# Optimization experiments

Hardware: AMD Instinct MI355X
Metric: run time of the kernel (lower is better)

The kernel has to match this reference:

```python
import jax, jax.numpy as jnp
import numpy as np

N, E, D = 20000, 640000, 128  # nodes, edges, hidden_nf
ED = 3  # edge_feat_nf (1 input col + distance col + geodesic col)
NORM_FACTOR = 100.0
NORM_CONST = 1.0
LN_EPS = 1e-5


def setup_inputs() -> dict:
    key = jax.random.key(0)
    ks = jax.random.split(key, 24)
    w = lambda k, s: (jax.random.normal(k, s, dtype=jnp.float32) * 0.1)
    inp = {
        "h": jax.random.normal(ks[0], (N, D), dtype=jnp.float32),
        "x": jax.random.normal(ks[1], (N, 3), dtype=jnp.float32),
        "edge_index": jax.random.randint(ks[2], (2, E), 0, N),
        "node_mask": jnp.ones((N, 1), jnp.float32),
        "edge_mask": jnp.ones((E, 1), jnp.float32),
        "edge_attr": jax.random.uniform(ks[3], (E, 1), dtype=jnp.float32),
        # GCLayer params
        "W_lin": w(ks[4], (D, D)), "b_lin": jnp.zeros((D,), jnp.float32),
        "We1": w(ks[5], (D + ED, D)), "be1": jnp.zeros((D,), jnp.float32),
        "We2": w(ks[6], (D, D)), "be2": jnp.zeros((D,), jnp.float32),
        "Wn1": w(ks[7], (D, D)), "bn1": jnp.zeros((D,), jnp.float32),
        "Wn2": w(ks[8], (D, D)), "bn2": jnp.zeros((D,), jnp.float32),
        "Wa1": w(ks[9], (2 * D + ED, D)), "ba1": jnp.zeros((D,), jnp.float32),
        "Wa2": w(ks[10], (D, 1)), "ba2": jnp.zeros((1,), jnp.float32),
        "ln_g": jnp.ones((D,), jnp.float32), "ln_b": jnp.zeros((D,), jnp.float32),
        # EquivariantUpdate coord_mlp params (last layer bias-free, gain 0.001)
        "Wc1": w(ks[11], (2 * D + ED, D)), "bc1": jnp.zeros((D,), jnp.float32),
        "Wc2": w(ks[12], (D, D)), "bc2": jnp.zeros((D,), jnp.float32),
        "Wc3": w(ks[13], (D, 1)) * 0.01,
    }
    return inp


def _forward(h, x, edge_index, node_mask, edge_mask, edge_attr,
             W_lin, b_lin, We1, be1, We2, be2, Wn1, bn1, Wn2, bn2,
             Wa1, ba1, Wa2, ba2, ln_g, ln_b, Wc1, bc1, Wc2, bc2, Wc3):
    silu = jax.nn.silu
    row, col = edge_index[0], edge_index[1]
    # coord2diff
    diff = x[row] - x[col]                                     # [E,3]
    radial = jnp.sum(diff * diff, axis=1, keepdims=True)
    dist = jnp.sqrt(radial + 1e-8)                             # [E,1]
    coord_diff = diff / (dist + NORM_CONST)
    e = jnp.concatenate([dist, edge_attr], axis=1)             # [E,2]
    # ---- GCLayer (Euclidean reduction of HGCLayer) ----
    hh = h @ W_lin + b_lin                                     # [N,D]
    hr, hc = hh[row], hh[col]
    geo = jnp.sqrt(jnp.sum((hr - hc) ** 2, axis=1, keepdims=True) + 1e-8)
    e3 = jnp.concatenate([e, geo], axis=1)                     # [E,3]
    att_in = jnp.concatenate([hr, hc, e3], axis=1)             # [E,2D+3]
    att = jax.nn.sigmoid(silu(att_in @ Wa1 + ba1) @ Wa2 + ba2) * edge_mask
    msg_in = jnp.concatenate([hc - hr, e3], axis=1)            # [E,D+3]
    msg = (silu(msg_in @ We1 + be1) @ We2 + be2) * att
    agg = jax.ops.segment_sum(msg, row, num_segments=hh.shape[0])  # [N,D]
    out = silu(agg @ Wn1 + bn1) @ Wn2 + bn2
    hh = hh + out
    mu = jnp.mean(hh, axis=-1, keepdims=True)
    var = jnp.mean((hh - mu) ** 2, axis=-1, keepdims=True)
    hh = (hh - mu) * jax.lax.rsqrt(var + LN_EPS) * ln_g + ln_b
    hh = silu(hh)
    # ---- EquivariantUpdate (tanh=False) ----
    cin = jnp.concatenate([hh[row], hh[col], e3], axis=1)      # [E,2D+3]
    m = silu(cin @ Wc1 + bc1)
    m = silu(m @ Wc2 + bc2)
    m = m @ Wc3                                                # [E,1]
    trans = coord_diff * m * edge_mask
    aggx = jax.ops.segment_sum(trans, row, num_segments=x.shape[0]) / NORM_FACTOR
    x_out = (x + aggx) * node_mask
    return hh, x_out


def reference(h, x, edge_index, node_mask, edge_mask, edge_attr,
              W_lin, b_lin, We1, be1, We2, be2, Wn1, bn1, Wn2, bn2,
              Wa1, ba1, Wa2, ba2, ln_g, ln_b, Wc1, bc1, Wc2, bc2, Wc3):
    return _forward(h, x, edge_index, node_mask, edge_mask, edge_attr,
                    W_lin, b_lin, We1, be1, We2, be2, Wn1, bn1, Wn2, bn2,
                    Wa1, ba1, Wa2, ba2, ln_g, ln_b, Wc1, bc1, Wc2, bc2, Wc3)
```

## Files before the change

### kernel.cpp

```cpp
#include <hip/hip_runtime.h>
#include <hip/hip_bf16.h>


#define D 128
#define RS 136

typedef unsigned short ushort;
typedef __fp16 half8 __attribute__((ext_vector_type(8)));
typedef __fp16 h16x2 __attribute__((ext_vector_type(2)));
typedef _Float16 f16x2 __attribute__((ext_vector_type(2)));
typedef __attribute__((ext_vector_type(4))) float f32x4;

__device__ __forceinline__ float rcpf(float x) { return __builtin_amdgcn_rcpf(x); }
__device__ __forceinline__ float siluf(float x) { return x * rcpf(1.0f + __expf(-x)); }
__device__ __forceinline__ float sigmf(float x) { return rcpf(1.0f + __expf(-x)); }
__device__ __forceinline__ ushort f2hs(float f) {
    _Float16 h = (_Float16)f; ushort u; __builtin_memcpy(&u, &h, 2); return u;
}
__device__ __forceinline__ unsigned pkh(float lo, float hi) {
    auto h = __builtin_amdgcn_cvt_pkrtz(lo, hi);
    unsigned u; __builtin_memcpy(&u, &h, 4); return u;
}
__device__ __forceinline__ float fdot2f(f16x2 a, f16x2 b, float c) {
#if __has_builtin(__builtin_amdgcn_fdot2)
    h16x2 ah, bh;
    __builtin_memcpy(&ah, &a, 4); __builtin_memcpy(&bh, &b, 4);
    return __builtin_amdgcn_fdot2(ah, bh, c, false);
#else
    return c + (float)a.x * (float)b.x + (float)a.y * (float)b.y;
#endif
}
#define MFMA16(a, b, c) __builtin_amdgcn_mfma_f32_16x16x32_f16((a), (b), (c), 0, 0, 0)

#define PWLIN 0
#define PWA1  5
#define PWE1  14
#define PWE2  19
#define PWN1  23
#define PWN2  28
#define PWC1  32
#define PWC2  41
#define NPACK 45

__global__ void k_zero(float* __restrict__ p, long n) {
    long i = (long)blockIdx.x * blockDim.x + threadIdx.x;
    long stride = (long)gridDim.x * blockDim.x;
    for (; i < n; i += stride) p[i] = 0.0f;
}

__global__ void k_hist(const int* __restrict__ eidx, int* __restrict__ cnt, int E) {
    int i = blockIdx.x * blockDim.x + threadIdx.x;
    const int stride = gridDim.x * blockDim.x;
    for (; i < E; i += stride) atomicAdd(&cnt[eidx[i]], 1);
}

__global__ __launch_bounds__(1024) void k_scan(const int* __restrict__ cnt,
                                               int* __restrict__ cur, int N) {
    __shared__ int part[1024];
    const int t = threadIdx.x;
    const int chunk = (N + 1023) / 1024;
    int s = 0;
    for (int k = 0; k < chunk; ++k) {
        const int i = t * chunk + k;
        if (i < N) s += cnt[i];
    }
    part[t] = s;
    __syncthreads();
    for (int d = 1; d < 1024; d <<= 1) {
        const int v = (t >= d) ? part[t - d] : 0;
        __syncthreads();
        part[t] += v;
        __syncthreads();
    }
    int base = (t == 0) ? 0 : part[t - 1];
    for (int k = 0; k < chunk; ++k) {
        const int i = t * chunk + k;
        if (i < N) { cur[i] = base; base += cnt[i]; }
    }
}

__global__ void k_scatter_build(
    const int* __restrict__ eidx, const float* __restrict__ x,
    const float* __restrict__ eattr, const float* __restrict__ emask,
    int* __restrict__ cur, float4* __restrict__ rec, int E) {
    int i = blockIdx.x * blockDim.x + threadIdx.x;
    const int stride = gridDim.x * blockDim.x;
    for (; i < E; i += stride) {
        const int r = eidx[i], c = eidx[E + i];
        const int p = atomicAdd(&cur[r], 1);
        const float dx = x[r * 3 + 0] - x[c * 3 + 0];
        const float dy = x[r * 3 + 1] - x[c * 3 + 1];
        const float dz = x[r * 3 + 2] - x[c * 3 + 2];
        const float dist = sqrtf(dx * dx + dy * dy + dz * dz + 1e-8f);
        const float inv = rcpf(dist + 1.0f);
        rec[2 * p + 0] = make_float4(__int_as_float(r), __int_as_float(c), dist, eattr[i]);
        rec[2 * p + 1] = make_float4(emask[i], dx * inv, dy * inv, dz * inv);
    }
}

__global__ __launch_bounds__(256) void k_packall(
    const float* __restrict__ W_lin, const float* __restrict__ b_lin,
    const float* __restrict__ Wa1, const float* __restrict__ ba1,
    const float* __restrict__ We1, const float* __restrict__ be1,
    const float* __restrict__ We2,
    const float* __restrict__ Wn1, const float* __restrict__ bn1,
    const float* __restrict__ Wn2,
    const float* __restrict__ Wc1, const float* __restrict__ bc1,
    const float* __restrict__ Wc2,
    ushort* __restrict__ pack) {
    const int b = blockIdx.x, t = threadIdx.x;
    const float* W = nullptr; const float* bias = nullptr;
    int kbase = 0, fold = 0, ext = 0, nW = 0;
    if (b < 5)       { W = W_lin; bias = b_lin; if (b == 4) { ext = 1; nW = 0; } else kbase = b * 32; }
    else if (b < 14) { int k = b - 5;  W = Wa1; bias = ba1; if (k == 8) { ext = 1; nW = 3; kbase = 256; } else { kbase = k * 32; fold = (k < 4); } }
    else if (b < 19) { int k = b - 14; W = We1; bias = be1; if (k == 4) { ext = 1; nW = 3; kbase = 128; } else kbase = k * 32; }
    else if (b < 23) { W = We2; kbase = (b - 19) * 32; }
    else if (b < 28) { int k = b - 23; W = Wn1; bias = bn1; if (k == 4) { ext = 1; nW = 0; } else kbase = k * 32; }
    else if (b < 32) { W = Wn2; kbase = (b - 28) * 32; }
    else if (b < 41) { int k = b - 32; W = Wc1; bias = bc1; if (k == 8) { ext = 1; nW = 3; kbase = 256; } else kbase = k * 32; }
    else             { W = Wc2; kbase = (b - 41) * 32; }
    ushort* dst = pack + (size_t)b * 4096;
#pragma unroll
    for (int i = 0; i < 16; ++i) {
        const int e = t + 256 * i;
        const int j = e & 7, lane = (e >> 3) & 63, nt = e >> 9;
        const int kl = (lane >> 4) * 8 + j;
        const int n = nt * 16 + (lane & 15);
        float v;
        if (!ext) {
            v = W[(kbase + kl) * D + n];
            if (fold) v += W[(kbase + kl + 128) * D + n];
        } else {
            v = (kl < nW) ? W[(kbase + kl) * D + n] : (kl == nW ? bias[n] : 0.0f);
        }
        dst[e] = f2hs(v);
    }
}

__global__ __launch_bounds__(256) void k_node_lin(
    const float* __restrict__ h, const ushort* __restrict__ pack,
    float* __restrict__ hh, ushort* __restrict__ hh1b, int N) {
    __shared__ ushort hs[64][RS];
    const int t = threadIdx.x, lane = t & 63, wave = t >> 6;
    const int quad = lane >> 4, l16 = lane & 15;
    const int mh = wave >> 1, nh = wave & 1;
    const int base = blockIdx.x * 64;

#pragma unroll
    for (int q = 0; q < 8; ++q) {
        const int f = t + 256 * q;
        const int row = f >> 5, c4 = (f & 31) << 2;
        const int node = base + row;
        float4 v = make_float4(0.f, 0.f, 0.f, 0.f);
        if (node < N) v = *(const float4*)(h + (size_t)node * D + c4);
        *(uint2*)&hs[row][c4] = make_uint2(pkh(v.x, v.y), pkh(v.z, v.w));
    }
    __syncthreads();

    half8 aext = (half8)0;
    if (quad == 0) aext[0] = (__fp16)1.0f;

    f32x4 acc[2][4] = {};
    const half8* pB = (const half8*)(pack + (size_t)PWLIN * 4096);
#pragma unroll
    for (int ks = 0; ks < 5; ++ks) {
        half8 bfr[4];
#pragma unroll
        for (int nt = 0; nt < 4; ++nt) bfr[nt] = pB[(ks * 8 + nh * 4 + nt) * 64 + lane];
#pragma unroll
        for (int mt = 0; mt < 2; ++mt) {
            const half8 a = (ks < 4) ? *(const half8*)&hs[mh * 32 + mt * 16 + l16][ks * 32 + quad * 8]
                                     : aext;
#pragma unroll
            for (int nt = 0; nt < 4; ++nt) acc[mt][nt] = MFMA16(a, bfr[nt], acc[mt][nt]);
        }
    }
#pragma unroll
    for (int mt = 0; mt < 2; ++mt)
#pragma unroll
        for (int reg = 0; reg < 4; ++reg) {
            const int g = base + mh * 32 + mt * 16 + quad * 4 + reg;
            if (g < N) {
#pragma unroll
                for (int nt = 0; nt < 4; ++nt) {
                    const int col = nh * 64 + nt * 16 + l16;
                    const float v = acc[mt][nt][reg];
                    hh[(size_t)g * D + col] = v;
                    hh1b[(size_t)g * D + col] = f2hs(v);
                }
            }
        }
}

__global__ __launch_bounds__(256, 4) void k_edge1(
    const float4* __restrict__ rec,
    const ushort* __restrict__ hh1b, const ushort* __restrict__ pack,
    const float* __restrict__ Wa2f, const float* __restrict__ ba2f,
    const float* __restrict__ be2f,
    float* __restrict__ agg, float* __restrict__ geo_c, int E) {
    __shared__ ushort ab_s[2][64][RS];
    __shared__ float dist_s[64], attr_s[64], geo_s[64], att_s[64], em_s[64];
    __shared__ int node_s[64], col_s[64];
    __shared__ float attp_s[4][64];

    float (*msg_s)[130] = (float(*)[130])&ab_s[0][0][0];

    const int t = threadIdx.x, lane = t & 63, w = t >> 6;
    const int quad = lane >> 4, l16 = lane & 15;
    const int base = blockIdx.x * 64;

    if (t < 64) {
        const int i = base + t;
        int r = 0, c = 0; float dist = 0.f, at = 0.f, emv = 0.f;
        if (i < E) {
            const float4 ra = rec[2 * i + 0];
            const float4 rb = rec[2 * i + 1];
            r = __float_as_int(ra.x); c = __float_as_int(ra.y);
            dist = ra.z; at = ra.w; emv = rb.x;
        }
        node_s[t] = r; col_s[t] = c;
        dist_s[t] = dist; attr_s[t] = at; em_s[t] = emv;
    }
    float wa2[2], b3[2];
#pragma unroll
    for (int nt = 0; nt < 2; ++nt) {
        const int col = w * 32 + nt * 16 + l16;
        wa2[nt] = Wa2f[col]; b3[nt] = be2f[col];
    }
    __syncthreads();

    {
        const int g = t >> 4;
#pragma unroll
        for (int it = 0; it < 4; ++it) {
            const int e = g * 4 + it;
            const uint4 vr = *(const uint4*)(hh1b + (size_t)node_s[e] * D + l16 * 8);
            const uint4 vc = *(const uint4*)(hh1b + (size_t)col_s[e] * D + l16 * 8);
            *(uint4*)&ab_s[0][e][l16 * 8] = vr;
            const unsigned* pr = (const unsigned*)&vr;
            const unsigned* pc = (const unsigned*)&vc;
            float s = 0.f; unsigned dw[4];
#pragma unroll
            for (int q = 0; q < 4; ++q) {
                f16x2 hr2, hc2;
                __builtin_memcpy(&hr2, &pr[q], 4);
                __builtin_memcpy(&hc2, &pc[q], 4);
                const f16x2 d2 = hc2 - hr2;
                __builtin_memcpy(&dw[q], &d2, 4);
                s = fdot2f(d2, d2, s);
            }
            *(uint4*)&ab_s[1][e][l16 * 8] = make_uint4(dw[0], dw[1], dw[2], dw[3]);
            s += __shfl_xor(s, 1); s += __shfl_xor(s, 2); s += __shfl_xor(s, 4); s += __shfl_xor(s, 8);
            if (l16 == 0) {
                const float gg = sqrtf(s + 1e-8f);
                geo_s[e] = gg;
                if (base + e < E) geo_c[base + e] = gg;
            }
        }
    }
    __syncthreads();

    half8 aext[4];
#pragma unroll
    for (int mt = 0; mt < 4; ++mt) {
        half8 v = (half8)0;
        if (quad == 0) {
            const int m = mt * 16 + l16;
            v[0] = (__fp16)dist_s[m]; v[1] = (__fp16)attr_s[m];
            v[2] = (__fp16)geo_s[m];  v[3] = (__fp16)1.0f;
        }
        aext[mt] = v;
    }

    f32x4 accA[4][2] = {}, accM[4][2] = {};
    {
        const half8* pA = (const half8*)(pack + (size_t)PWA1 * 4096);
        const half8* pM = (const half8*)(pack + (size_t)PWE1 * 4096);
#pragma unroll
        for (int ks = 0; ks < 9; ++ks) {
            const half8 bA0 = pA[(ks * 8 + w * 2 + 0) * 64 + lane];
            const half8 bA1 = pA[(ks * 8 + w * 2 + 1) * 64 + lane];
            half8 bM0 = (half8)0, bM1 = (half8)0;
            if (ks >= 4) {
                bM0 = pM[((ks - 4) * 8 + w * 2 + 0) * 64 + lane];
                bM1 = pM[((ks - 4) * 8 + w * 2 + 1) * 64 + lane];
            }
#pragma unroll
            for (int mt = 0; mt < 4; ++mt) {
                const half8 a = (ks < 4) ? *(const half8*)&ab_s[0][mt * 16 + l16][ks * 32 + quad * 8]
                              : (ks < 8) ? *(const half8*)&ab_s[1][mt * 16 + l16][(ks - 4) * 32 + quad * 8]
                                         : aext[mt];
                accA[mt][0] = MFMA16(a, bA0, accA[mt][0]);
                accA[mt][1] = MFMA16(a, bA1, accA[mt][1]);
                if (ks >= 4) {
                    accM[mt][0] = MFMA16(a, bM0, accM[mt][0]);
                    accM[mt][1] = MFMA16(a, bM1, accM[mt][1]);
                }
            }
        }
    }
#pragma unroll
    for (int mt = 0; mt < 4; ++mt)
#pragma unroll
        for (int reg = 0; reg < 4; ++reg) {
            float p = siluf(accA[mt][0][reg]) * wa2[0] + siluf(accA[mt][1][reg]) * wa2[1];
            p += __shfl_xor(p, 1); p += __shfl_xor(p, 2); p += __shfl_xor(p, 4); p += __shfl_xor(p, 8);
            if (l16 == 0) attp_s[w][mt * 16 + quad * 4 + reg] = p;
        }
    __syncthreads();

    if (t < 64)
        att_s[t] = sigmf(attp_s[0][t] + attp_s[1][t] + attp_s[2][t] + attp_s[3][t] + ba2f[0]) * em_s[t];
#pragma unroll
    for (int mt = 0; mt < 4; ++mt)
#pragma unroll
        for (int reg = 0; reg < 4; ++reg) {
            const int row = mt * 16 + quad * 4 + reg;
#pragma unroll
            for (int nt = 0; nt < 2; ++nt)
                ab_s[0][row][w * 32 + nt * 16 + l16] = f2hs(siluf(accM[mt][nt][reg]));
        }
    __syncthreads();

    f32x4 acc3[4][2] = {};
    {
        const half8* pB = (const half8*)(pack + (size_t)PWE2 * 4096);
#pragma unroll
        for (int ks = 0; ks < 4; ++ks) {
            const half8 b0 = pB[(ks * 8 + w * 2 + 0) * 64 + lane];
            const half8 b1 = pB[(ks * 8 + w * 2 + 1) * 64 + lane];
#pragma unroll
            for (int mt = 0; mt < 4; ++mt) {
                const half8 a = *(const half8*)&ab_s[0][mt * 16 + l16][ks * 32 + quad * 8];
                acc3[mt][0] = MFMA16(a, b0, acc3[mt][0]);
                acc3[mt][1] = MFMA16(a, b1, acc3[mt][1]);
            }
        }
    }
    __syncthreads();
#pragma unroll
    for (int mt = 0; mt < 4; ++mt)
#pragma unroll
        for (int reg = 0; reg < 4; ++reg) {
            const int row = mt * 16 + quad * 4 + reg;
            const float av = att_s[row];
#pragma unroll
            for (int nt = 0; nt < 2; ++nt)
                msg_s[row][w * 32 + nt * 16 + l16] = (acc3[mt][nt][reg] + b3[nt]) * av;
        }
    __syncthreads();

    {
        const int j = t & 127, h = t >> 7;
        const int r0 = node_s[h * 32];
        if (r0 == node_s[h * 32 + 31]) {
            float acc = 0.f;
#pragma unroll
            for (int k = 0; k < 32; ++k) acc += msg_s[h * 32 + k][j];
            atomicAdd(&agg[(size_t)r0 * D + j], acc);
        } else {
            float acc = 0.f;
            int rprev = r0;
#pragma unroll
            for (int k = 0; k < 32; ++k) {
                const int row = h * 32 + k;
                const int rn = node_s[row];
                if (rn != rprev) {
                    atomicAdd(&agg[(size_t)rprev * D + j], acc);
                    acc = 0.f; rprev = rn;
                }
                acc += msg_s[row][j];
            }
            atomicAdd(&agg[(size_t)rprev * D + j], acc);
        }
    }
}

__global__ __launch_bounds__(256) void k_node2(
    const float* __restrict__ agg, float* hio,
    const ushort* __restrict__ pack,
    const float* __restrict__ bn2f,
    const float* __restrict__ ln_g, const float* __restrict__ ln_b,
    ushort* __restrict__ hh2b, int N) {
    __shared__ ushort ag_s[64][RS];
    __shared__ float redS[2][64], redQ[2][64];
    const int t = threadIdx.x, lane = t & 63, wave = t >> 6;
    const int quad = lane >> 4, l16 = lane & 15;
    const int mh = wave >> 1, nh = wave & 1;
    const int base = blockIdx.x * 64;

#pragma unroll
    for (int q = 0; q < 8; ++q) {
        const int f = t + 256 * q;
        const int row = f >> 5, c4 = (f & 31) << 2;
        const int node = base + row;
        float4 v = make_float4(0.f, 0.f, 0.f, 0.f);
        if (node < N) v = *(const float4*)(agg + (size_t)node * D + c4);
        *(uint2*)&ag_s[row][c4] = make_uint2(pkh(v.x, v.y), pkh(v.z, v.w));
    }
    float bn2[4], lg[4], lb[4];
#pragma unroll
    for (int nt = 0; nt < 4; ++nt) {
        const int col = nh * 64 + nt * 16 + l16;
        bn2[nt] = bn2f[col]; lg[nt] = ln_g[col]; lb[nt] = ln_b[col];
    }
    __syncthreads();

    half8 aext = (half8)0;
    if (quad == 0) aext[0] = (__fp16)1.0f;

    f32x4 acc[2][4] = {};
    {
        const half8* pB = (const half8*)(pack + (size_t)PWN1 * 4096);
#pragma unroll
        for (int ks = 0; ks < 5; ++ks) {
            half8 bfr[4];
#pragma unroll
            for (int nt = 0; nt < 4; ++nt) bfr[nt] = pB[(ks * 8 + nh * 4 + nt) * 64 + lane];
#pragma unroll
            for (int mt = 0; mt < 2; ++mt) {
                const half8 a = (ks < 4) ? *(const half8*)&ag_s[mh * 32 + mt * 16 + l16][ks * 32 + quad * 8]
                                         : aext;
#pragma unroll
                for (int nt = 0; nt < 4; ++nt) acc[mt][nt] = MFMA16(a, bfr[nt], acc[mt][nt]);
            }
        }
    }
    __syncthreads();
#pragma unroll
    for (int mt = 0; mt < 2; ++mt)
#pragma unroll
        for (int reg = 0; reg < 4; ++reg) {
            const int row = mh * 32 + mt * 16 + quad * 4 + reg;
#pragma unroll
            for (int nt = 0; nt < 4; ++nt)
                ag_s[row][nh * 64 + nt * 16 + l16] = f2hs(siluf(acc[mt][nt][reg]));
        }
    __syncthreads();

    {
        const half8* pB = (const half8*)(pack + (size_t)PWN2 * 4096);
#pragma unroll
        for (int mt = 0; mt < 2; ++mt)
#pragma unroll
            for (int nt = 0; nt < 4; ++nt) acc[mt][nt] = (f32x4)0.0f;
#pragma unroll
        for (int ks = 0; ks < 4; ++ks) {
            half8 bfr[4];
#pragma unroll
            for (int nt = 0; nt < 4; ++nt) bfr[nt] = pB[(ks * 8 + nh * 4 + nt) * 64 + lane];
#pragma unroll
            for (int mt = 0; mt < 2; ++mt) {
                const half8 a = *(const half8*)&ag_s[mh * 32 + mt * 16 + l16][ks * 32 + quad * 8];
#pragma unroll
                for (int nt = 0; nt < 4; ++nt) acc[mt][nt] = MFMA16(a, bfr[nt], acc[mt][nt]);
            }
        }
    }
#pragma unroll
    for (int mt = 0; mt < 2; ++mt)
#pragma unroll
        for (int reg = 0; reg < 4; ++reg) {
            const int row = mh * 32 + mt * 16 + quad * 4 + reg;
            const int g = base + row;
            float s = 0.f, qq = 0.f;
#pragma unroll
            for (int nt = 0; nt < 4; ++nt) {
                const int col = nh * 64 + nt * 16 + l16;
                float v = acc[mt][nt][reg] + bn2[nt];
                if (g < N) v += hio[(size_t)g * D + col];
                acc[mt][nt][reg] = v;
                s += v; qq += v * v;
            }
            s += __shfl_xor(s, 1); s += __shfl_xor(s, 2); s += __shfl_xor(s, 4); s += __shfl_xor(s, 8);
            qq += __shfl_xor(qq, 1); qq += __shfl_xor(qq, 2); qq += __shfl_xor(qq, 4); qq += __shfl_xor(qq, 8);
            if (l16 == 0) { redS[nh][row] = s; redQ[nh][row] = qq; }
        }
    __syncthreads();

#pragma unroll
    for (int mt = 0; mt < 2; ++mt)
#pragma unroll
        for (int reg = 0; reg < 4; ++reg) {
            const int row = mh * 32 + mt * 16 + quad * 4 + reg;
            const int g = base + row;
            const float mu = (redS[0][row] + redS[1][row]) * (1.0f / D);
            const float var = (redQ[0][row] + redQ[1][row]) * (1.0f / D) - mu * mu;
            const float rstd = rsqrtf(var + 1e-5f);
            if (g < N) {
#pragma unroll
                for (int nt = 0; nt < 4; ++nt) {
                    const int col = nh * 64 + nt * 16 + l16;
                    const float hn = (acc[mt][nt][reg] - mu) * rstd * lg[nt] + lb[nt];
                    const float o = siluf(hn);
                    hio[(size_t)g * D + col] = o;
                    hh2b[(size_t)g * D + col] = f2hs(o);
                }
            }
        }
}

__global__ __launch_bounds__(256, 4) void k_edge2(
    const float4* __restrict__ rec, const float* __restrict__ geo_c,
    const ushort* __restrict__ hh2b, const ushort* __restrict__ pack,
    const float* __restrict__ bc2f, const float* __restrict__ Wc3f,
    float* __restrict__ aggx, int E) {
    __shared__ ushort ar_s[64][RS];
    __shared__ ushort ac_s[64][RS];
    __shared__ float dist_s[64], attr_s[64], geo_s[64], tr_s[64];
    __shared__ float cdx_s[64], cdy_s[64], cdz_s[64];
    __shared__ int node_s[64], col_s[64];
    __shared__ float mp_s[4][64];

    const int t = threadIdx.x, lane = t & 63, w = t >> 6;
    const int quad = lane >> 4, l16 = lane & 15;
    const int base = blockIdx.x * 64;

    if (t < 64) {
        const int i = base + t;
        int r = 0, c = 0;
        float dist = 1.f, geo = 0.f, at = 0.f, emv = 0.f, cdx = 0.f, cdy = 0.f, cdz = 0.f;
        if (i < E) {
            const float4 ra = rec[2 * i + 0];
            const float4 rb = rec[2 * i + 1];
            r = __float_as_int(ra.x); c = __float_as_int(ra.y);
            dist = ra.z; at = ra.w;
            emv = rb.x; cdx = rb.y; cdy = rb.z; cdz = rb.w;
            geo = geo_c[i];
        }
        node_s[t] = r; col_s[t] = c;
        dist_s[t] = dist; geo_s[t] = geo; attr_s[t] = at; tr_s[t] = emv;
        cdx_s[t] = cdx; cdy_s[t] = cdy; cdz_s[t] = cdz;
    }
    float bc2[2], wc3[2];
#pragma unroll
    for (int nt = 0; nt < 2; ++nt) {
        const int col = w * 32 + nt * 16 + l16;
        bc2[nt] = bc2f[col]; wc3[nt] = Wc3f[col];
    }
    __syncthreads();

    {
        const int g = t >> 4;
#pragma unroll
        for (int it = 0; it < 4; ++it) {
            const int e = g * 4 + it;
            *(uint4*)&ar_s[e][l16 * 8] = *(const uint4*)(hh2b + (size_t)node_s[e] * D + l16 * 8);
            *(uint4*)&ac_s[e][l16 * 8] = *(const uint4*)(hh2b + (size_t)col_s[e] * D + l16 * 8);
        }
    }
    __syncthreads();

    half8 aext[4];
#pragma unroll
    for (int mt = 0; mt < 4; ++mt) {
        half8 v = (half8)0;
        if (quad == 0) {
            const int m = mt * 16 + l16;
            v[0] = (__fp16)dist_s[m]; v[1] = (__fp16)attr_s[m];
            v[2] = (__fp16)geo_s[m];  v[3] = (__fp16)1.0f;
        }
        aext[mt] = v;
    }

    {
        f32x4 acc[4][2] = {};
        const half8* pB = (const half8*)(pack + (size_t)PWC1 * 4096);
#pragma unroll
        for (int ks = 0; ks < 9; ++ks) {
            const half8 b0 = pB[(ks * 8 + w * 2 + 0) * 64 + lane];
            const half8 b1 = pB[(ks * 8 + w * 2 + 1) * 64 + lane];
#pragma unroll
            for (int mt = 0; mt < 4; ++mt) {
                const half8 a = (ks < 4) ? *(const half8*)&ar_s[mt * 16 + l16][ks * 32 + quad * 8]
                              : (ks < 8) ? *(const half8*)&ac_s[mt * 16 + l16][(ks - 4) * 32 + quad * 8]
                                         : aext[mt];
                acc[mt][0] = MFMA16(a, b0, acc[mt][0]);
                acc[mt][1] = MFMA16(a, b1, acc[mt][1]);
            }
        }
        __syncthreads();
#pragma unroll
        for (int mt = 0; mt < 4; ++mt)
#pragma unroll
            for (int reg = 0; reg < 4; ++reg) {
                const int row = mt * 16 + quad * 4 + reg;
#pragma unroll
                for (int nt = 0; nt < 2; ++nt)
                    ar_s[row][w * 32 + nt * 16 + l16] = f2hs(siluf(acc[mt][nt][reg]));
            }
    }
    __syncthreads();

    {
        f32x4 acc[4][2] = {};
        const half8* pB = (const half8*)(pack + (size_t)PWC2 * 4096);
#pragma unroll
        for (int ks = 0; ks < 4; ++ks) {
            const half8 b0 = pB[(ks * 8 + w * 2 + 0) * 64 + lane];
            const half8 b1 = pB[(ks * 8 + w * 2 + 1) * 64 + lane];
#pragma unroll
            for (int mt = 0; mt < 4; ++mt) {
                const half8 a = *(const half8*)&ar_s[mt * 16 + l16][ks * 32 + quad * 8];
                acc[mt][0] = MFMA16(a, b0, acc[mt][0]);
                acc[mt][1] = MFMA16(a, b1, acc[mt][1]);
            }
        }
#pragma unroll
        for (int mt = 0; mt < 4; ++mt)
#pragma unroll
            for (int reg = 0; reg < 4; ++reg) {
                float p = siluf(acc[mt][0][reg] + bc2[0]) * wc3[0]
                        + siluf(acc[mt][1][reg] + bc2[1]) * wc3[1];
                p += __shfl_xor(p, 1); p += __shfl_xor(p, 2); p += __shfl_xor(p, 4); p += __shfl_xor(p, 8);
                if (l16 == 0) mp_s[w][mt * 16 + quad * 4 + reg] = p;
            }
    }
    __syncthreads();

    if (t < 64) {
        const float m = mp_s[0][t] + mp_s[1][t] + mp_s[2][t] + mp_s[3][t];
        tr_s[t] = m * tr_s[t];
        if (base + t >= E) tr_s[t] = 0.f;
    }
    __syncthreads();

    {
        const int h = t >> 7, tt = t & 127;
        if (tt < 3) {
            const float* cds = (tt == 0) ? cdx_s : (tt == 1) ? cdy_s : cdz_s;
            float acc = 0.f;
            int rprev = node_s[h * 32];
#pragma unroll
            for (int k = 0; k < 32; ++k) {
                const int row = h * 32 + k;
                const int rn = node_s[row];
                if (rn != rprev) {
                    atomicAdd(&aggx[rprev * 4 + tt], acc);
                    acc = 0.f; rprev = rn;
                }
                acc += cds[row] * tr_s[row];
            }
            atomicAdd(&aggx[rprev * 4 + tt], acc);
        }
    }
}

__global__ void k_coord(const float* __restrict__ x, const float* __restrict__ nmask,
                        const float* __restrict__ aggx, float* __restrict__ out_x, int N) {
    const int idx = blockIdx.x * blockDim.x + threadIdx.x;
    if (idx >= N * 3) return;
    const int i = idx / 3, d = idx - i * 3;
    out_x[idx] = (x[idx] + aggx[i * 4 + d] * (1.0f / 100.0f)) * nmask[i];
}

extern "C" void kernel_launch(void* const* d_in, const int* in_sizes, int n_in,
                              void* d_out, int out_size, void* d_ws, size_t ws_size,
                              hipStream_t stream) {
    const float* h     = (const float*)d_in[0];
    const float* x     = (const float*)d_in[1];
    const int*   eidx  = (const int*)d_in[2];
    const float* nmask = (const float*)d_in[3];
    const float* emask = (const float*)d_in[4];
    const float* eattr = (const float*)d_in[5];
    const float* W_lin = (const float*)d_in[6];
    const float* b_lin = (const float*)d_in[7];
    const float* We1   = (const float*)d_in[8];
    const float* be1   = (const float*)d_in[9];
    const float* We2   = (const float*)d_in[10];
    const float* be2   = (const float*)d_in[11];
    const float* Wn1   = (const float*)d_in[12];
    const float* bn1   = (const float*)d_in[13];
    const float* Wn2   = (const float*)d_in[14];
    const float* bn2   = (const float*)d_in[15];
    const float* Wa1   = (const float*)d_in[16];
    const float* ba1   = (const float*)d_in[17];
    const float* Wa2   = (const float*)d_in[18];
    const float* ba2   = (const float*)d_in[19];
    const float* ln_g  = (const float*)d_in[20];
    const float* ln_b  = (const float*)d_in[21];
    const float* Wc1   = (const float*)d_in[22];
    const float* bc1   = (const float*)d_in[23];
    const float* Wc2   = (const float*)d_in[24];
    const float* bc2   = (const float*)d_in[25];
    const float* Wc3   = (const float*)d_in[26];

    const int N = in_sizes[0] / D;
    const int E = in_sizes[2] / 2;

    char* wp = (char*)d_ws;
    auto take = [&](size_t bytes) -> void* {
        void* p = wp; wp += (bytes + 255) & ~(size_t)255; return p;
    };
    float*  agg   = (float*)take((size_t)N * D * 4);
    float*  aggx  = (float*)take((size_t)N * 4 * 4);
    int*    cnt   = (int*)take((size_t)N * 4);
    int*    cur   = (int*)take((size_t)N * 4);
    float4* rec   = (float4*)take((size_t)E * 32);
    float*  geo_c = (float*)take((size_t)E * 4);
    ushort* hh1b  = (ushort*)take((size_t)N * D * 2);
    ushort* hh2b  = (ushort*)take((size_t)N * D * 2);
    ushort* pack  = (ushort*)take((size_t)NPACK * 4096 * 2);

    float* out_h = (float*)d_out;
    float* out_x = out_h + (size_t)N * D;

    const int EB = (E + 63) / 64;
    const int NB = (N + 63) / 64;
    const long zn = ((char*)(cnt + N) - (char*)agg) / 4;

    k_zero<<<2048, 256, 0, stream>>>(agg, zn);
    k_packall<<<NPACK, 256, 0, stream>>>(W_lin, b_lin, Wa1, ba1, We1, be1, We2,
                                         Wn1, bn1, Wn2, Wc1, bc1, Wc2, pack);
    k_hist<<<1024, 256, 0, stream>>>(eidx, cnt, E);
    k_scan<<<1, 1024, 0, stream>>>(cnt, cur, N);
    k_scatter_build<<<1024, 256, 0, stream>>>(eidx, x, eattr, emask, cur, rec, E);
    k_node_lin<<<NB, 256, 0, stream>>>(h, pack, out_h, hh1b, N);
    k_edge1<<<EB, 256, 0, stream>>>(rec, hh1b, pack, Wa2, ba2, be2, agg, geo_c, E);
    k_node2<<<NB, 256, 0, stream>>>(agg, out_h, pack, bn2, ln_g, ln_b, hh2b, N);
    k_edge2<<<EB, 256, 0, stream>>>(rec, geo_c, hh2b, pack, bc2, Wc3, aggx, E);
    k_coord<<<(N * 3 + 255) / 256, 256, 0, stream>>>(x, nmask, aggx, out_x, N);
}
```

Baseline: 535.9 us.

## Hoist first-layer edge matmuls to per-node projections gathered per edge

The first linear layers of the edge attention, edge message and coordinate MLPs are split by linearity into per-node projections (U, V, M for edge1 and P, Q for edge2), computed once per node in the node kernels with MFMA. The edge kernels then gather those projected rows, add the small edge-feature terms from weights staged in shared memory, and apply the activation, so the large per-edge K=256+ matmuls are replaced by elementwise work. This moves matmul FLOPs from E edges to N nodes, at the cost of extra node-side outputs, more gather bandwidth (several fp16/fp32 rows per edge), and extra fp16 rounding of differences. Occupancy hints for the edge kernels are raised to 6 blocks per SM.

```diff
diff --git a/kernel.cpp b/kernel.cpp
--- a/kernel.cpp
+++ b/kernel.cpp
@@ -20,6 +20,14 @@
 __device__ __forceinline__ unsigned pkh(float lo, float hi) {
     auto h = __builtin_amdgcn_cvt_pkrtz(lo, hi);
     unsigned u; __builtin_memcpy(&u, &h, 4); return u;
+}
+__device__ __forceinline__ unsigned pksub(unsigned a, unsigned b) {
+    f16x2 x, y; __builtin_memcpy(&x, &a, 4); __builtin_memcpy(&y, &b, 4);
+    f16x2 d = x - y; unsigned r; __builtin_memcpy(&r, &d, 4); return r;
+}
+__device__ __forceinline__ float2 up2(unsigned u) {
+    f16x2 h; __builtin_memcpy(&h, &u, 4);
+    return make_float2((float)h.x, (float)h.y);
 }
 __device__ __forceinline__ float fdot2f(f16x2 a, f16x2 b, float c) {
 #if __has_builtin(__builtin_amdgcn_fdot2)
@@ -33,14 +41,16 @@
 #define MFMA16(a, b, c) __builtin_amdgcn_mfma_f32_16x16x32_f16((a), (b), (c), 0, 0, 0)
 
 #define PWLIN 0
-#define PWA1  5
-#define PWE1  14
-#define PWE2  19
-#define PWN1  23
-#define PWN2  28
-#define PWC1  32
-#define PWC2  41
-#define NPACK 45
+#define PU    5
+#define PV    9
+#define PM    13
+#define PE2   17
+#define PN1   21
+#define PN2   26
+#define PP    30
+#define PQ    34
+#define PC2   38
+#define NPACK 42
 
 __global__ void k_zero(float* __restrict__ p, long n) {
     long i = (long)blockIdx.x * blockDim.x + threadIdx.x;
@@ -100,25 +110,27 @@
 
 __global__ __launch_bounds__(256) void k_packall(
     const float* __restrict__ W_lin, const float* __restrict__ b_lin,
-    const float* __restrict__ Wa1, const float* __restrict__ ba1,
-    const float* __restrict__ We1, const float* __restrict__ be1,
+    const float* __restrict__ Wa1,
+    const float* __restrict__ We1,
     const float* __restrict__ We2,
     const float* __restrict__ Wn1, const float* __restrict__ bn1,
     const float* __restrict__ Wn2,
-    const float* __restrict__ Wc1, const float* __restrict__ bc1,
+    const float* __restrict__ Wc1,
     const float* __restrict__ Wc2,
     ushort* __restrict__ pack) {
     const int b = blockIdx.x, t = threadIdx.x;
     const float* W = nullptr; const float* bias = nullptr;
     int kbase = 0, fold = 0, ext = 0, nW = 0;
     if (b < 5)       { W = W_lin; bias = b_lin; if (b == 4) { ext = 1; nW = 0; } else kbase = b * 32; }
-    else if (b < 14) { int k = b - 5;  W = Wa1; bias = ba1; if (k == 8) { ext = 1; nW = 3; kbase = 256; } else { kbase = k * 32; fold = (k < 4); } }
-    else if (b < 19) { int k = b - 14; W = We1; bias = be1; if (k == 4) { ext = 1; nW = 3; kbase = 128; } else kbase = k * 32; }
-    else if (b < 23) { W = We2; kbase = (b - 19) * 32; }
-    else if (b < 28) { int k = b - 23; W = Wn1; bias = bn1; if (k == 4) { ext = 1; nW = 0; } else kbase = k * 32; }
-    else if (b < 32) { W = Wn2; kbase = (b - 28) * 32; }
-    else if (b < 41) { int k = b - 32; W = Wc1; bias = bc1; if (k == 8) { ext = 1; nW = 3; kbase = 256; } else kbase = k * 32; }
-    else             { W = Wc2; kbase = (b - 41) * 32; }
+    else if (b < 9)  { W = Wa1; kbase = (b - 5) * 32; fold = 1; }
+    else if (b < 13) { W = Wa1; kbase = 128 + (b - 9) * 32; }
+    else if (b < 17) { W = We1; kbase = (b - 13) * 32; }
+    else if (b < 21) { W = We2; kbase = (b - 17) * 32; }
+    else if (b < 26) { int k = b - 21; W = Wn1; bias = bn1; if (k == 4) { ext = 1; nW = 0; } else kbase = k * 32; }
+    else if (b < 30) { W = Wn2; kbase = (b - 26) * 32; }
+    else if (b < 34) { W = Wc1; kbase = (b - 30) * 32; }
+    else if (b < 38) { W = Wc1; kbase = 128 + (b - 34) * 32; }
+    else             { W = Wc2; kbase = (b - 38) * 32; }
     ushort* dst = pack + (size_t)b * 4096;
 #pragma unroll
     for (int i = 0; i < 16; ++i) {
@@ -139,7 +151,9 @@
 
 __global__ __launch_bounds__(256) void k_node_lin(
     const float* __restrict__ h, const ushort* __restrict__ pack,
-    float* __restrict__ hh, ushort* __restrict__ hh1b, int N) {
+    float* __restrict__ hh, ushort* __restrict__ hh1b,
+    float* __restrict__ Uf, ushort* __restrict__ Vh, ushort* __restrict__ Mh,
+    const float* __restrict__ ba1f, int N) {
     __shared__ ushort hs[64][RS];
     const int t = threadIdx.x, lane = t & 63, wave = t >> 6;
     const int quad = lane >> 4, l16 = lane & 15;
@@ -155,55 +169,150 @@
         if (node < N) v = *(const float4*)(h + (size_t)node * D + c4);
         *(uint2*)&hs[row][c4] = make_uint2(pkh(v.x, v.y), pkh(v.z, v.w));
     }
+    float ba1v[4];
+#pragma unroll
+    for (int nt = 0; nt < 4; ++nt) ba1v[nt] = ba1f[nh * 64 + nt * 16 + l16];
     __syncthreads();
 
     half8 aext = (half8)0;
     if (quad == 0) aext[0] = (__fp16)1.0f;
 
     f32x4 acc[2][4] = {};
-    const half8* pB = (const half8*)(pack + (size_t)PWLIN * 4096);
-#pragma unroll
-    for (int ks = 0; ks < 5; ++ks) {
-        half8 bfr[4];
-#pragma unroll
-        for (int nt = 0; nt < 4; ++nt) bfr[nt] = pB[(ks * 8 + nh * 4 + nt) * 64 + lane];
-#pragma unroll
-        for (int mt = 0; mt < 2; ++mt) {
-            const half8 a = (ks < 4) ? *(const half8*)&hs[mh * 32 + mt * 16 + l16][ks * 32 + quad * 8]
-                                     : aext;
-#pragma unroll
-            for (int nt = 0; nt < 4; ++nt) acc[mt][nt] = MFMA16(a, bfr[nt], acc[mt][nt]);
-        }
-    }
+    {
+        const half8* pB = (const half8*)(pack + (size_t)PWLIN * 4096);
+#pragma unroll
+        for (int ks = 0; ks < 5; ++ks) {
+            half8 bfr[4];
+#pragma unroll
+            for (int nt = 0; nt < 4; ++nt) bfr[nt] = pB[(ks * 8 + nh * 4 + nt) * 64 + lane];
+#pragma unroll
+            for (int mt = 0; mt < 2; ++mt) {
+                const half8 a = (ks < 4) ? *(const half8*)&hs[mh * 32 + mt * 16 + l16][ks * 32 + quad * 8]
+                                         : aext;
+#pragma unroll
+                for (int nt = 0; nt < 4; ++nt) acc[mt][nt] = MFMA16(a, bfr[nt], acc[mt][nt]);
+            }
+        }
+    }
+    __syncthreads();
 #pragma unroll
     for (int mt = 0; mt < 2; ++mt)
 #pragma unroll
         for (int reg = 0; reg < 4; ++reg) {
-            const int g = base + mh * 32 + mt * 16 + quad * 4 + reg;
-            if (g < N) {
-#pragma unroll
-                for (int nt = 0; nt < 4; ++nt) {
-                    const int col = nh * 64 + nt * 16 + l16;
-                    const float v = acc[mt][nt][reg];
+            const int row = mh * 32 + mt * 16 + quad * 4 + reg;
+            const int g = base + row;
+#pragma unroll
+            for (int nt = 0; nt < 4; ++nt) {
+                const int col = nh * 64 + nt * 16 + l16;
+                const float v = acc[mt][nt][reg];
+                const ushort hv = f2hs(v);
+                hs[row][col] = hv;
+                if (g < N) {
                     hh[(size_t)g * D + col] = v;
-                    hh1b[(size_t)g * D + col] = f2hs(v);
+                    hh1b[(size_t)g * D + col] = hv;
                 }
             }
         }
-}
-
-__global__ __launch_bounds__(256, 4) void k_edge1(
+    __syncthreads();
+
+    {
+        f32x4 a2[2][4] = {};
+        const half8* pB = (const half8*)(pack + (size_t)PU * 4096);
+#pragma unroll
+        for (int ks = 0; ks < 4; ++ks) {
+            half8 bfr[4];
+#pragma unroll
+            for (int nt = 0; nt < 4; ++nt) bfr[nt] = pB[(ks * 8 + nh * 4 + nt) * 64 + lane];
+#pragma unroll
+            for (int mt = 0; mt < 2; ++mt) {
+                const half8 a = *(const half8*)&hs[mh * 32 + mt * 16 + l16][ks * 32 + quad * 8];
+#pragma unroll
+                for (int nt = 0; nt < 4; ++nt) a2[mt][nt] = MFMA16(a, bfr[nt], a2[mt][nt]);
+            }
+        }
+#pragma unroll
+        for (int mt = 0; mt < 2; ++mt)
+#pragma unroll
+            for (int reg = 0; reg < 4; ++reg) {
+                const int g = base + mh * 32 + mt * 16 + quad * 4 + reg;
+                if (g < N)
+#pragma unroll
+                    for (int nt = 0; nt < 4; ++nt)
+                        Uf[(size_t)g * D + nh * 64 + nt * 16 + l16] = a2[mt][nt][reg] + ba1v[nt];
+            }
+    }
+    {
+        f32x4 a2[2][4] = {};
+        const half8* pB = (const half8*)(pack + (size_t)PV * 4096);
+#pragma unroll
+        for (int ks = 0; ks < 4; ++ks) {
+            half8 bfr[4];
+#pragma unroll
+            for (int nt = 0; nt < 4; ++nt) bfr[nt] = pB[(ks * 8 + nh * 4 + nt) * 64 + lane];
+#pragma unroll
+            for (int mt = 0; mt < 2; ++mt) {
+                const half8 a = *(const half8*)&hs[mh * 32 + mt * 16 + l16][ks * 32 + quad * 8];
+#pragma unroll
+                for (int nt = 0; nt < 4; ++nt) a2[mt][nt] = MFMA16(a, bfr[nt], a2[mt][nt]);
+            }
+        }
+#pragma unroll
+        for (int mt = 0; mt < 2; ++mt)
+#pragma unroll
+            for (int reg = 0; reg < 4; ++reg) {
+                const int g = base + mh * 32 + mt * 16 + quad * 4 + reg;
+                if (g < N)
+#pragma unroll
+                    for (int nt = 0; nt < 4; ++nt)
+                        Vh[(size_t)g * D + nh * 64 + nt * 16 + l16] = f2hs(a2[mt][nt][reg]);
+            }
+    }
+    {
+        f32x4 a2[2][4] = {};
+        const half8* pB = (const half8*)(pack + (size_t)PM * 4096);
+#pragma unroll
+        for (int ks = 0; ks < 4; ++ks) {
+            half8 bfr[4];
+#pragma unroll
+            for (int nt = 0; nt < 4; ++nt) bfr[nt] = pB[(ks * 8 + nh * 4 + nt) * 64 + lane];
+#pragma unroll
+            for (int mt = 0; mt < 2; ++mt) {
+                const half8 a = *(const half8*)&hs[mh * 32 + mt * 16 + l16][ks * 32 + quad * 8];
+#pragma unroll
+                for (int nt = 0; nt < 4; ++nt) a2[mt][nt] = MFMA16(a, bfr[nt], a2[mt][nt]);
+            }
+        }
+#pragma unroll
+        for (int mt = 0; mt < 2; ++mt)
+#pragma unroll
+            for (int reg = 0; reg < 4; ++reg) {
+                const int g = base + mh * 32 + mt * 16 + quad * 4 + reg;
+                if (g < N)
+#pragma unroll
+                    for (int nt = 0; nt < 4; ++nt)
+                        Mh[(size_t)g * D + nh * 64 + nt * 16 + l16] = f2hs(a2[mt][nt][reg]);
+            }
+    }
+}
+
+__global__ __launch_bounds__(256, 6) void k_edge1(
     const float4* __restrict__ rec,
-    const ushort* __restrict__ hh1b, const ushort* __restrict__ pack,
+    const ushort* __restrict__ hh1b,
+    const float*  __restrict__ Uf,
+    const ushort* __restrict__ Vh,
+    const ushort* __restrict__ Mh,
+    const ushort* __restrict__ pack,
+    const float* __restrict__ Wa1, const float* __restrict__ We1,
+    const float* __restrict__ be1f,
     const float* __restrict__ Wa2f, const float* __restrict__ ba2f,
     const float* __restrict__ be2f,
     float* __restrict__ agg, float* __restrict__ geo_c, int E) {
-    __shared__ ushort ab_s[2][64][RS];
+    __shared__ ushort m1_s[64][RS];
+    __shared__ float ew_s[7][128];
     __shared__ float dist_s[64], attr_s[64], geo_s[64], att_s[64], em_s[64];
     __shared__ int node_s[64], col_s[64];
-    __shared__ float attp_s[4][64];
-
-    float (*msg_s)[130] = (float(*)[130])&ab_s[0][0][0];
+
+    float (*msg_s)[RS] = (float(*)[RS])&m1_s[0][0];
 
     const int t = threadIdx.x, lane = t & 63, w = t >> 6;
     const int quad = lane >> 4, l16 = lane & 15;
@@ -221,12 +330,17 @@
         node_s[t] = r; col_s[t] = c;
         dist_s[t] = dist; attr_s[t] = at; em_s[t] = emv;
     }
-    float wa2[2], b3[2];
-#pragma unroll
-    for (int nt = 0; nt < 2; ++nt) {
-        const int col = w * 32 + nt * 16 + l16;
-        wa2[nt] = Wa2f[col]; b3[nt] = be2f[col];
-    }
+    for (int i = t; i < 896; i += 256) {
+        const int r = i >> 7, c = i & 127;
+        float v;
+        if (r < 3)      v = Wa1[(256 + r) * D + c];
+        else if (r < 6) v = We1[(128 + (r - 3)) * D + c];
+        else            v = be1f[c];
+        ew_s[r][c] = v;
+    }
+    float b3[2];
+#pragma unroll
+    for (int nt = 0; nt < 2; ++nt) b3[nt] = be2f[w * 32 + nt * 16 + l16];
     __syncthreads();
 
     {
@@ -236,20 +350,17 @@
             const int e = g * 4 + it;
             const uint4 vr = *(const uint4*)(hh1b + (size_t)node_s[e] * D + l16 * 8);
             const uint4 vc = *(const uint4*)(hh1b + (size_t)col_s[e] * D + l16 * 8);
-            *(uint4*)&ab_s[0][e][l16 * 8] = vr;
             const unsigned* pr = (const unsigned*)&vr;
             const unsigned* pc = (const unsigned*)&vc;
-            float s = 0.f; unsigned dw[4];
+            float s = 0.f;
 #pragma unroll
             for (int q = 0; q < 4; ++q) {
                 f16x2 hr2, hc2;
                 __builtin_memcpy(&hr2, &pr[q], 4);
                 __builtin_memcpy(&hc2, &pc[q], 4);
                 const f16x2 d2 = hc2 - hr2;
-                __builtin_memcpy(&dw[q], &d2, 4);
                 s = fdot2f(d2, d2, s);
             }
-            *(uint4*)&ab_s[1][e][l16 * 8] = make_uint4(dw[0], dw[1], dw[2], dw[3]);
             s += __shfl_xor(s, 1); s += __shfl_xor(s, 2); s += __shfl_xor(s, 4); s += __shfl_xor(s, 8);
             if (l16 == 0) {
                 const float gg = sqrtf(s + 1e-8f);
@@ -260,119 +371,100 @@
     }
     __syncthreads();
 
-    half8 aext[4];
-#pragma unroll
-    for (int mt = 0; mt < 4; ++mt) {
-        half8 v = (half8)0;
-        if (quad == 0) {
-            const int m = mt * 16 + l16;
-            v[0] = (__fp16)dist_s[m]; v[1] = (__fp16)attr_s[m];
-            v[2] = (__fp16)geo_s[m];  v[3] = (__fp16)1.0f;
-        }
-        aext[mt] = v;
-    }
-
-    f32x4 accA[4][2] = {}, accM[4][2] = {};
-    {
-        const half8* pA = (const half8*)(pack + (size_t)PWA1 * 4096);
-        const half8* pM = (const half8*)(pack + (size_t)PWE1 * 4096);
-#pragma unroll
-        for (int ks = 0; ks < 9; ++ks) {
-            const half8 bA0 = pA[(ks * 8 + w * 2 + 0) * 64 + lane];
-            const half8 bA1 = pA[(ks * 8 + w * 2 + 1) * 64 + lane];
-            half8 bM0 = (half8)0, bM1 = (half8)0;
-            if (ks >= 4) {
-                bM0 = pM[((ks - 4) * 8 + w * 2 + 0) * 64 + lane];
-                bM1 = pM[((ks - 4) * 8 + w * 2 + 1) * 64 + lane];
-            }
-#pragma unroll
-            for (int mt = 0; mt < 4; ++mt) {
-                const half8 a = (ks < 4) ? *(const half8*)&ab_s[0][mt * 16 + l16][ks * 32 + quad * 8]
-                              : (ks < 8) ? *(const half8*)&ab_s[1][mt * 16 + l16][(ks - 4) * 32 + quad * 8]
-                                         : aext[mt];
-                accA[mt][0] = MFMA16(a, bA0, accA[mt][0]);
-                accA[mt][1] = MFMA16(a, bA1, accA[mt][1]);
-                if (ks >= 4) {
-                    accM[mt][0] = MFMA16(a, bM0, accM[mt][0]);
-                    accM[mt][1] = MFMA16(a, bM1, accM[mt][1]);
-                }
-            }
-        }
-    }
-#pragma unroll
-    for (int mt = 0; mt < 4; ++mt)
-#pragma unroll
-        for (int reg = 0; reg < 4; ++reg) {
-            float p = siluf(accA[mt][0][reg]) * wa2[0] + siluf(accA[mt][1][reg]) * wa2[1];
-            p += __shfl_xor(p, 1); p += __shfl_xor(p, 2); p += __shfl_xor(p, 4); p += __shfl_xor(p, 8);
-            if (l16 == 0) attp_s[w][mt * 16 + quad * 4 + reg] = p;
-        }
-    __syncthreads();
-
-    if (t < 64)
-        att_s[t] = sigmf(attp_s[0][t] + attp_s[1][t] + attp_s[2][t] + attp_s[3][t] + ba2f[0]) * em_s[t];
-#pragma unroll
-    for (int mt = 0; mt < 4; ++mt)
-#pragma unroll
-        for (int reg = 0; reg < 4; ++reg) {
-            const int row = mt * 16 + quad * 4 + reg;
-#pragma unroll
-            for (int nt = 0; nt < 2; ++nt)
-                ab_s[0][row][w * 32 + nt * 16 + l16] = f2hs(siluf(accM[mt][nt][reg]));
-        }
+    {
+        const int row = t >> 2, cq = t & 3;
+        const int nr = node_s[row], nc = col_s[row];
+        const float dist = dist_s[row], attr = attr_s[row], geo = geo_s[row];
+        const float*  pU  = Uf + (size_t)nr * D + cq * 32;
+        const ushort* pVr = Vh + (size_t)nr * D + cq * 32;
+        const ushort* pVc = Vh + (size_t)nc * D + cq * 32;
+        const ushort* pMr = Mh + (size_t)nr * D + cq * 32;
+        const ushort* pMc = Mh + (size_t)nc * D + cq * 32;
+        float p = 0.f;
+#pragma unroll
+        for (int k4 = 0; k4 < 8; ++k4) {
+            const int c4 = cq * 32 + k4 * 4;
+            const float4 u  = *(const float4*)(pU + k4 * 4);
+            const uint2 vru = *(const uint2*)(pVr + k4 * 4);
+            const uint2 vcu = *(const uint2*)(pVc + k4 * 4);
+            const uint2 mru = *(const uint2*)(pMr + k4 * 4);
+            const uint2 mcu = *(const uint2*)(pMc + k4 * 4);
+            const float2 vd01 = up2(pksub(vcu.x, vru.x));
+            const float2 vd23 = up2(pksub(vcu.y, vru.y));
+            const float2 md01 = up2(pksub(mcu.x, mru.x));
+            const float2 md23 = up2(pksub(mcu.y, mru.y));
+            const float4 e0 = *(const float4*)&ew_s[0][c4];
+            const float4 e1 = *(const float4*)&ew_s[1][c4];
+            const float4 e2 = *(const float4*)&ew_s[2][c4];
+            const float4 f0 = *(const float4*)&ew_s[3][c4];
+            const float4 f1 = *(const float4*)&ew_s[4][c4];
+            const float4 f2 = *(const float4*)&ew_s[5][c4];
+            const float4 bb = *(const float4*)&ew_s[6][c4];
+            const float4 w2 = *(const float4*)(Wa2f + c4);
+            const float a0 = u.x + vd01.x + dist * e0.x + attr * e1.x + geo * e2.x;
+            const float a1 = u.y + vd01.y + dist * e0.y + attr * e1.y + geo * e2.y;
+            const float a2 = u.z + vd23.x + dist * e0.z + attr * e1.z + geo * e2.z;
+            const float a3 = u.w + vd23.y + dist * e0.w + attr * e1.w + geo * e2.w;
+            p += siluf(a0) * w2.x + siluf(a1) * w2.y + siluf(a2) * w2.z + siluf(a3) * w2.w;
+            const float m0 = siluf(md01.x + dist * f0.x + attr * f1.x + geo * f2.x + bb.x);
+            const float m1v = siluf(md01.y + dist * f0.y + attr * f1.y + geo * f2.y + bb.y);
+            const float m2 = siluf(md23.x + dist * f0.z + attr * f1.z + geo * f2.z + bb.z);
+            const float m3 = siluf(md23.y + dist * f0.w + attr * f1.w + geo * f2.w + bb.w);
+            *(uint2*)&m1_s[row][c4] = make_uint2(pkh(m0, m1v), pkh(m2, m3));
+        }
+        p += __shfl_xor(p, 1); p += __shfl_xor(p, 2);
+        if (cq == 0) att_s[row] = sigmf(p + ba2f[0]) * em_s[row];
+    }
     __syncthreads();
 
     f32x4 acc3[4][2] = {};
     {
-        const half8* pB = (const half8*)(pack + (size_t)PWE2 * 4096);
+        const half8* pB = (const half8*)(pack + (size_t)PE2 * 4096);
 #pragma unroll
         for (int ks = 0; ks < 4; ++ks) {
             const half8 b0 = pB[(ks * 8 + w * 2 + 0) * 64 + lane];
             const half8 b1 = pB[(ks * 8 + w * 2 + 1) * 64 + lane];
 #pragma unroll
             for (int mt = 0; mt < 4; ++mt) {
-                const half8 a = *(const half8*)&ab_s[0][mt * 16 + l16][ks * 32 + quad * 8];
+                const half8 a = *(const half8*)&m1_s[mt * 16 + l16][ks * 32 + quad * 8];
                 acc3[mt][0] = MFMA16(a, b0, acc3[mt][0]);
                 acc3[mt][1] = MFMA16(a, b1, acc3[mt][1]);
             }
         }
     }
     __syncthreads();
-#pragma unroll
-    for (int mt = 0; mt < 4; ++mt)
-#pragma unroll
-        for (int reg = 0; reg < 4; ++reg) {
-            const int row = mt * 16 + quad * 4 + reg;
-            const float av = att_s[row];
-#pragma unroll
-            for (int nt = 0; nt < 2; ++nt)
-                msg_s[row][w * 32 + nt * 16 + l16] = (acc3[mt][nt][reg] + b3[nt]) * av;
-        }
-    __syncthreads();
-
-    {
-        const int j = t & 127, h = t >> 7;
-        const int r0 = node_s[h * 32];
-        if (r0 == node_s[h * 32 + 31]) {
+
+#pragma unroll
+    for (int pass = 0; pass < 2; ++pass) {
+#pragma unroll
+        for (int mt = 0; mt < 2; ++mt)
+#pragma unroll
+            for (int reg = 0; reg < 4; ++reg) {
+                const int row = (pass * 2 + mt) * 16 + quad * 4 + reg;
+                const float av = att_s[row];
+#pragma unroll
+                for (int nt = 0; nt < 2; ++nt)
+                    msg_s[row - pass * 32][w * 32 + nt * 16 + l16] =
+                        (acc3[pass * 2 + mt][nt][reg] + b3[nt]) * av;
+            }
+        __syncthreads();
+        {
+            const int j = t & 127, s = t >> 7;
+            const int r0 = pass * 32 + s * 16;
             float acc = 0.f;
-#pragma unroll
-            for (int k = 0; k < 32; ++k) acc += msg_s[h * 32 + k][j];
-            atomicAdd(&agg[(size_t)r0 * D + j], acc);
-        } else {
-            float acc = 0.f;
-            int rprev = r0;
-#pragma unroll
-            for (int k = 0; k < 32; ++k) {
-                const int row = h * 32 + k;
-                const int rn = node_s[row];
+            int rprev = node_s[r0];
+#pragma unroll
+            for (int k = 0; k < 16; ++k) {
+                const int rn = node_s[r0 + k];
                 if (rn != rprev) {
                     atomicAdd(&agg[(size_t)rprev * D + j], acc);
                     acc = 0.f; rprev = rn;
                 }
-                acc += msg_s[row][j];
+                acc += msg_s[s * 16 + k][j];
             }
             atomicAdd(&agg[(size_t)rprev * D + j], acc);
         }
+        __syncthreads();
     }
 }
 
@@ -381,7 +473,8 @@
     const ushort* __restrict__ pack,
     const float* __restrict__ bn2f,
     const float* __restrict__ ln_g, const float* __restrict__ ln_b,
-    ushort* __restrict__ hh2b, int N) {
+    const float* __restrict__ bc1f,
+    ushort* __restrict__ Ph, ushort* __restrict__ Qh, int N) {
     __shared__ ushort ag_s[64][RS];
     __shared__ float redS[2][64], redQ[2][64];
     const int t = threadIdx.x, lane = t & 63, wave = t >> 6;
@@ -398,11 +491,11 @@
         if (node < N) v = *(const float4*)(agg + (size_t)node * D + c4);
         *(uint2*)&ag_s[row][c4] = make_uint2(pkh(v.x, v.y), pkh(v.z, v.w));
     }
-    float bn2[4], lg[4], lb[4];
+    float bn2[4], lg[4], lb[4], bc1v[4];
 #pragma unroll
     for (int nt = 0; nt < 4; ++nt) {
         const int col = nh * 64 + nt * 16 + l16;
-        bn2[nt] = bn2f[col]; lg[nt] = ln_g[col]; lb[nt] = ln_b[col];
+        bn2[nt] = bn2f[col]; lg[nt] = ln_g[col]; lb[nt] = ln_b[col]; bc1v[nt] = bc1f[col];
     }
     __syncthreads();
 
@@ -411,7 +504,7 @@
 
     f32x4 acc[2][4] = {};
     {
-        const half8* pB = (const half8*)(pack + (size_t)PWN1 * 4096);
+        const half8* pB = (const half8*)(pack + (size_t)PN1 * 4096);
 #pragma unroll
         for (int ks = 0; ks < 5; ++ks) {
             half8 bfr[4];
@@ -439,7 +532,7 @@
     __syncthreads();
 
     {
-        const half8* pB = (const half8*)(pack + (size_t)PWN2 * 4096);
+        const half8* pB = (const half8*)(pack + (size_t)PN2 * 4096);
 #pragma unroll
         for (int mt = 0; mt < 2; ++mt)
 #pragma unroll
@@ -487,26 +580,80 @@
             const float mu = (redS[0][row] + redS[1][row]) * (1.0f / D);
             const float var = (redQ[0][row] + redQ[1][row]) * (1.0f / D) - mu * mu;
             const float rstd = rsqrtf(var + 1e-5f);
-            if (g < N) {
-#pragma unroll
-                for (int nt = 0; nt < 4; ++nt) {
-                    const int col = nh * 64 + nt * 16 + l16;
-                    const float hn = (acc[mt][nt][reg] - mu) * rstd * lg[nt] + lb[nt];
-                    const float o = siluf(hn);
-                    hio[(size_t)g * D + col] = o;
-                    hh2b[(size_t)g * D + col] = f2hs(o);
-                }
-            }
-        }
-}
-
-__global__ __launch_bounds__(256, 4) void k_edge2(
+#pragma unroll
+            for (int nt = 0; nt < 4; ++nt) {
+                const int col = nh * 64 + nt * 16 + l16;
+                const float hn = (acc[mt][nt][reg] - mu) * rstd * lg[nt] + lb[nt];
+                const float o = siluf(hn);
+                ag_s[row][col] = f2hs(o);
+                if (g < N) hio[(size_t)g * D + col] = o;
+            }
+        }
+    __syncthreads();
+
+    {
+        f32x4 a2[2][4] = {};
+        const half8* pB = (const half8*)(pack + (size_t)PP * 4096);
+#pragma unroll
+        for (int ks = 0; ks < 4; ++ks) {
+            half8 bfr[4];
+#pragma unroll
+            for (int nt = 0; nt < 4; ++nt) bfr[nt] = pB[(ks * 8 + nh * 4 + nt) * 64 + lane];
+#pragma unroll
+            for (int mt = 0; mt < 2; ++mt) {
+                const half8 a = *(const half8*)&ag_s[mh * 32 + mt * 16 + l16][ks * 32 + quad * 8];
+#pragma unroll
+                for (int nt = 0; nt < 4; ++nt) a2[mt][nt] = MFMA16(a, bfr[nt], a2[mt][nt]);
+            }
+        }
+#pragma unroll
+        for (int mt = 0; mt < 2; ++mt)
+#pragma unroll
+            for (int reg = 0; reg < 4; ++reg) {
+                const int g = base + mh * 32 + mt * 16 + quad * 4 + reg;
+                if (g < N)
+#pragma unroll
+                    for (int nt = 0; nt < 4; ++nt)
+                        Ph[(size_t)g * D + nh * 64 + nt * 16 + l16] = f2hs(a2[mt][nt][reg] + bc1v[nt]);
+            }
+    }
+    {
+        f32x4 a2[2][4] = {};
+        const half8* pB = (const half8*)(pack + (size_t)PQ * 4096);
+#pragma unroll
+        for (int ks = 0; ks < 4; ++ks) {
+            half8 bfr[4];
+#pragma unroll
+            for (int nt = 0; nt < 4; ++nt) bfr[nt] = pB[(ks * 8 + nh * 4 + nt) * 64 + lane];
+#pragma unroll
+            for (int mt = 0; mt < 2; ++mt) {
+                const half8 a = *(const half8*)&ag_s[mh * 32 + mt * 16 + l16][ks * 32 + quad * 8];
+#pragma unroll
+                for (int nt = 0; nt < 4; ++nt) a2[mt][nt] = MFMA16(a, bfr[nt], a2[mt][nt]);
+            }
+        }
+#pragma unroll
+        for (int mt = 0; mt < 2; ++mt)
+#pragma unroll
+            for (int reg = 0; reg < 4; ++reg) {
+                const int g = base + mh * 32 + mt * 16 + quad * 4 + reg;
+                if (g < N)
+#pragma unroll
+                    for (int nt = 0; nt < 4; ++nt)
+                        Qh[(size_t)g * D + nh * 64 + nt * 16 + l16] = f2hs(a2[mt][nt][reg]);
+            }
+    }
+}
+
+__global__ __launch_bounds__(256, 6) void k_edge2(
     const float4* __restrict__ rec, const float* __restrict__ geo_c,
-    const ushort* __restrict__ hh2b, const ushort* __restrict__ pack,
+    const ushort* __restrict__ Ph, const ushort* __restrict__ Qh,
+    const ushort* __restrict__ pack,
+    const float* __restrict__ Wc1,
     const float* __restrict__ bc2f, const float* __restrict__ Wc3f,
     float* __restrict__ aggx, int E) {
-    __shared__ ushort ar_s[64][RS];
-    __shared__ ushort ac_s[64][RS];
+    __shared__ ushort c1_s[64][RS];
+    __shared__ float ew_s[3][128];
     __shared__ float dist_s[64], attr_s[64], geo_s[64], tr_s[64];
     __shared__ float cdx_s[64], cdy_s[64], cdz_s[64];
     __shared__ int node_s[64], col_s[64];
@@ -532,6 +679,10 @@
         dist_s[t] = dist; geo_s[t] = geo; attr_s[t] = at; tr_s[t] = emv;
         cdx_s[t] = cdx; cdy_s[t] = cdy; cdz_s[t] = cdz;
     }
+    for (int i = t; i < 384; i += 256) {
+        const int r = i >> 7, c = i & 127;
+        ew_s[r][c] = Wc1[(256 + r) * D + c];
+    }
     float bc2[2], wc3[2];
 #pragma unroll
     for (int nt = 0; nt < 2; ++nt) {
@@ -541,67 +692,40 @@
     __syncthreads();
 
     {
-        const int g = t >> 4;
-#pragma unroll
-        for (int it = 0; it < 4; ++it) {
-            const int e = g * 4 + it;
-            *(uint4*)&ar_s[e][l16 * 8] = *(const uint4*)(hh2b + (size_t)node_s[e] * D + l16 * 8);
-            *(uint4*)&ac_s[e][l16 * 8] = *(const uint4*)(hh2b + (size_t)col_s[e] * D + l16 * 8);
-        }
-    }
-    __syncthreads();
-
-    half8 aext[4];
-#pragma unroll
-    for (int mt = 0; mt < 4; ++mt) {
-        half8 v = (half8)0;
-        if (quad == 0) {
-            const int m = mt * 16 + l16;
-            v[0] = (__fp16)dist_s[m]; v[1] = (__fp16)attr_s[m];
-            v[2] = (__fp16)geo_s[m];  v[3] = (__fp16)1.0f;
-        }
-        aext[mt] = v;
-    }
+        const int row = t >> 2, cq = t & 3;
+        const int nr = node_s[row], nc = col_s[row];
+        const float dist = dist_s[row], attr = attr_s[row], geo = geo_s[row];
+        const ushort* pP = Ph + (size_t)nr * D + cq * 32;
+        const ushort* pQ = Qh + (size_t)nc * D + cq * 32;
+#pragma unroll
+        for (int k4 = 0; k4 < 8; ++k4) {
+            const int c4 = cq * 32 + k4 * 4;
+            const uint2 pu = *(const uint2*)(pP + k4 * 4);
+            const uint2 qu = *(const uint2*)(pQ + k4 * 4);
+            const float2 p01 = up2(pu.x), p23 = up2(pu.y);
+            const float2 q01 = up2(qu.x), q23 = up2(qu.y);
+            const float4 e0 = *(const float4*)&ew_s[0][c4];
+            const float4 e1 = *(const float4*)&ew_s[1][c4];
+            const float4 e2 = *(const float4*)&ew_s[2][c4];
+            const float c0 = siluf(p01.x + q01.x + dist * e0.x + attr * e1.x + geo * e2.x);
+            const float c1 = siluf(p01.y + q01.y + dist * e0.y + attr * e1.y + geo * e2.y);
+            const float c2 = siluf(p23.x + q23.x + dist * e0.z + attr * e1.z + geo * e2.z);
+            const float c3 = siluf(p23.y + q23.y + dist * e0.w + attr * e1.w + geo * e2.w);
+            *(uint2*)&c1_s[row][c4] = make_uint2(pkh(c0, c1), pkh(c2, c3));
+        }
+    }
+    __syncthreads();
 
     {
         f32x4 acc[4][2] = {};
-        const half8* pB = (const half8*)(pack + (size_t)PWC1 * 4096);
-#pragma unroll
-        for (int ks = 0; ks < 9; ++ks) {
-            const half8 b0 = pB[(ks * 8 + w * 2 + 0) * 64 + lane];
-            const half8 b1 = pB[(ks * 8 + w * 2 + 1) * 64 + lane];
-#pragma unroll
-            for (int mt = 0; mt < 4; ++mt) {
-                const half8 a = (ks < 4) ? *(const half8*)&ar_s[mt * 16 + l16][ks * 32 + quad * 8]
-                              : (ks < 8) ? *(const half8*)&ac_s[mt * 16 + l16][(ks - 4) * 32 + quad * 8]
-                                         : aext[mt];
-                acc[mt][0] = MFMA16(a, b0, acc[mt][0]);
-                acc[mt][1] = MFMA16(a, b1, acc[mt][1]);
-            }
-        }
-        __syncthreads();
-#pragma unroll
-        for (int mt = 0; mt < 4; ++mt)
-#pragma unroll
-            for (int reg = 0; reg < 4; ++reg) {
-                const int row = mt * 16 + quad * 4 + reg;
-#pragma unroll
-                for (int nt = 0; nt < 2; ++nt)
-                    ar_s[row][w * 32 + nt * 16 + l16] = f2hs(siluf(acc[mt][nt][reg]));
-            }
-    }
-    __syncthreads();
-
-    {
-        f32x4 acc[4][2] = {};
-        const half8* pB = (const half8*)(pack + (size_t)PWC2 * 4096);
+        const half8* pB = (const half8*)(pack + (size_t)PC2 * 4096);
 #pragma unroll
         for (int ks = 0; ks < 4; ++ks) {
             const half8 b0 = pB[(ks * 8 + w * 2 + 0) * 64 + lane];
             const half8 b1 = pB[(ks * 8 + w * 2 + 1) * 64 + lane];
 #pragma unroll
             for (int mt = 0; mt < 4; ++mt) {
-                const half8 a = *(const half8*)&ar_s[mt * 16 + l16][ks * 32 + quad * 8];
+                const half8 a = *(const half8*)&c1_s[mt * 16 + l16][ks * 32 + quad * 8];
                 acc[mt][0] = MFMA16(a, b0, acc[mt][0]);
                 acc[mt][1] = MFMA16(a, b1, acc[mt][1]);
             }
@@ -699,7 +823,11 @@
     float4* rec   = (float4*)take((size_t)E * 32);
     float*  geo_c = (float*)take((size_t)E * 4);
     ushort* hh1b  = (ushort*)take((size_t)N * D * 2);
-    ushort* hh2b  = (ushort*)take((size_t)N * D * 2);
+    float*  Uf    = (float*)take((size_t)N * D * 4);
+    ushort* Vh    = (ushort*)take((size_t)N * D * 2);
+    ushort* Mh    = (ushort*)take((size_t)N * D * 2);
+    ushort* Ph    = (ushort*)take((size_t)N * D * 2);
+    ushort* Qh    = (ushort*)take((size_t)N * D * 2);
     ushort* pack  = (ushort*)take((size_t)NPACK * 4096 * 2);
 
     float* out_h = (float*)d_out;
@@ -710,14 +838,15 @@
     const long zn = ((char*)(cnt + N) - (char*)agg) / 4;
 
     k_zero<<<2048, 256, 0, stream>>>(agg, zn);
-    k_packall<<<NPACK, 256, 0, stream>>>(W_lin, b_lin, Wa1, ba1, We1, be1, We2,
-                                         Wn1, bn1, Wn2, Wc1, bc1, Wc2, pack);
+    k_packall<<<NPACK, 256, 0, stream>>>(W_lin, b_lin, Wa1, We1, We2,
+                                         Wn1, bn1, Wn2, Wc1, Wc2, pack);
     k_hist<<<1024, 256, 0, stream>>>(eidx, cnt, E);
     k_scan<<<1, 1024, 0, stream>>>(cnt, cur, N);
     k_scatter_build<<<1024, 256, 0, stream>>>(eidx, x, eattr, emask, cur, rec, E);
-    k_node_lin<<<NB, 256, 0, stream>>>(h, pack, out_h, hh1b, N);
-    k_edge1<<<EB, 256, 0, stream>>>(rec, hh1b, pack, Wa2, ba2, be2, agg, geo_c, E);
-    k_node2<<<NB, 256, 0, stream>>>(agg, out_h, pack, bn2, ln_g, ln_b, hh2b, N);
-    k_edge2<<<EB, 256, 0, stream>>>(rec, geo_c, hh2b, pack, bc2, Wc3, aggx, E);
+    k_node_lin<<<NB, 256, 0, stream>>>(h, pack, out_h, hh1b, Uf, Vh, Mh, ba1, N);
+    k_edge1<<<EB, 256, 0, stream>>>(rec, hh1b, Uf, Vh, Mh, pack, Wa1, We1, be1,
+                                    Wa2, ba2, be2, agg, geo_c, E);
+    k_node2<<<NB, 256, 0, stream>>>(agg, out_h, pack, bn2, ln_g, ln_b, bc1, Ph, Qh, N);
+    k_edge2<<<EB, 256, 0, stream>>>(rec, geo_c, Ph, Qh, pack, Wc1, bc2, Wc3, aggx, E);
     k_coord<<<(N * 3 + 255) / 256, 256, 0, stream>>>(x, nmask, aggx, out_x, N);
 }
```

New measurement: 493.0 us. 8.0% less time.
